# Kernel optimization log

Measured on AMD Instinct MI355X. Metric: run time of the kernel, lower is better.

## Reference

```python
import jax, jax.numpy as jnp
import numpy as np

B, S, D, H = 4, 2048, 1024, 16
HD = D // H

def setup_inputs() -> dict:
    key = jax.random.key(0)
    ks = jax.random.split(key, 11)
    s = 1.0 / np.sqrt(D)
    return {
        "query": jax.random.normal(ks[0], (B, S, D), jnp.float32),
        "key_": jax.random.normal(ks[1], (B, S, D), jnp.float32),
        "value": jax.random.normal(ks[2], (B, S, D), jnp.float32),
        "Wq": jax.random.normal(ks[3], (D, D), jnp.float32) * s,
        "bq": jax.random.normal(ks[4], (D,), jnp.float32) * s,
        "Wk": jax.random.normal(ks[5], (D, D), jnp.float32) * s,
        "bk": jax.random.normal(ks[6], (D,), jnp.float32) * s,
        "Wv": jax.random.normal(ks[7], (D, D), jnp.float32) * s,
        "bv": jax.random.normal(ks[8], (D,), jnp.float32) * s,
        "Wo": jax.random.normal(ks[9], (D, D), jnp.float32) * s,
        "bo": jax.random.normal(ks[10], (D,), jnp.float32) * s,
    }

def reference(query, key_, value, Wq, bq, Wk, bk, Wv, bv, Wo, bo):
    # projections (torch Linear: x @ W.T + b)
    q = query @ Wq.T + bq
    k = key_ @ Wk.T + bk
    v = value @ Wv.T + bv
    # [B,S,D] -> [B,H,S,hd]
    q = q.reshape(B, S, H, HD).transpose(0, 2, 1, 3)
    k = k.reshape(B, S, H, HD).transpose(0, 2, 1, 3)
    v = v.reshape(B, S, H, HD).transpose(0, 2, 1, 3)
    scale = HD ** 0.5
    scores = jnp.einsum('bhqd,bhkd->bhqk', q, k) / scale
    attn = jax.nn.softmax(scores, axis=-1)
    out = jnp.einsum('bhqk,bhkd->bhqd', attn, v)
    out = out.transpose(0, 2, 1, 3).reshape(B, S, D)
    return out @ Wo.T + bo
```

## Files before the change

kernel.cpp:

```cpp
#include <hip/hip_runtime.h>
#include <math.h>

#define B_ 4
#define S_ 2048
#define D_ 1024
#define H_ 16
#define HD_ 64
#define M_ (B_*S_)
#define BH_ (B_*H_)

typedef __attribute__((ext_vector_type(4))) float f32x4;
typedef _Float16 f16;
typedef __attribute__((ext_vector_type(8))) _Float16 f16x8;
typedef __attribute__((ext_vector_type(2))) __fp16 fp16x2_raw;
typedef unsigned short u16;

#define QSCALE 0.18033688011112042f

__device__ __forceinline__ unsigned pkh(float a, float b) {
    fp16x2_raw h = __builtin_amdgcn_cvt_pkrtz(a, b);
    unsigned r; __builtin_memcpy(&r, &h, 4);
    return r;
}
__device__ __forceinline__ uint2 f4_to_h4(float4 v) {
    uint2 r;
    r.x = pkh(v.x, v.y);
    r.y = pkh(v.z, v.w);
    return r;
}
__device__ __forceinline__ void gload_lds16(const void* g, void* l) {
    __builtin_amdgcn_global_load_lds(
        (const __attribute__((address_space(1))) void*)g,
        (__attribute__((address_space(3))) void*)l, 16, 0, 0);
}
#define MFMA16(a,b,c) __builtin_amdgcn_mfma_f32_16x16x32_f16((a),(b),(c),0,0,0)

__global__ __launch_bounds__(256) void conv_w_kernel(
    const float* __restrict__ w0, const float* __restrict__ w1,
    const float* __restrict__ w2, const float* __restrict__ w3,
    f16* __restrict__ out)
{
    const float* src = (blockIdx.y==0)?w0:(blockIdx.y==1)?w1:(blockIdx.y==2)?w2:w3;
    size_t off = (size_t)blockIdx.y << 20;
    size_t i = ((size_t)blockIdx.x*256 + threadIdx.x)*4;
    float4 v = *(const float4*)&src[i];
    *(uint2*)&out[off + i] = f4_to_h4(v);
}

__global__ __launch_bounds__(256) void conv_in_kernel(
    const float* __restrict__ src, f16* __restrict__ out)
{
    size_t i = ((size_t)blockIdx.x*256 + threadIdx.x)*4;
    float4 v = *(const float4*)&src[i];
    *(uint2*)&out[i] = f4_to_h4(v);
}

template<int MODE>
__global__ __launch_bounds__(256, 2) void gemm_mfma(
    const f16* __restrict__ Af16,
    const f16* __restrict__ Wh16,
    const float* __restrict__ bias,
    void* out0)
{
    __shared__ u16 Ah[128][32];
    __shared__ u16 Bh[128][32];

    const int t = threadIdx.x;
    const int lane = t & 63;
    const int w = t >> 6;
    const int wm = w >> 1, wn = w & 1;
    const int m0 = (int)(blockIdx.x >> 3) * 128;
    const int n0 = (int)(blockIdx.x & 7) * 128;

    const int srow_base = w*32;
    const int lrow_off  = lane >> 2;
    const int k8        = (lane & 3) * 8;

    f32x4 acc[4][4];
    #pragma unroll
    for (int i = 0; i < 4; ++i)
        #pragma unroll
        for (int j = 0; j < 4; ++j) { f32x4 z = {0.f,0.f,0.f,0.f}; acc[i][j] = z; }

    for (int k0 = 0; k0 < D_; k0 += 32) {
        __syncthreads();
        #pragma unroll
        for (int c = 0; c < 2; ++c) {
            int lrow = srow_base + c*16;
            int row = lrow + lrow_off;
            int kw = k8 ^ ((row & 3) << 3);
            size_t asrc;
            if constexpr (MODE == 3) {
                int m = m0 + row;
                int b = m >> 11, s = m & 2047;
                int kk = k0 + kw;
                asrc = (((size_t)b*H_ + (kk >> 6))*S_ + s)*HD_ + (kk & 63);
            } else {
                asrc = (size_t)(m0 + row)*D_ + k0 + kw;
            }
            gload_lds16(&Af16[asrc], &Ah[lrow][0]);
            gload_lds16(&Wh16[(size_t)(n0 + row)*D_ + k0 + kw], &Bh[lrow][0]);
        }
        __syncthreads();

        f16x8 ah[4], bh4[4];
        #pragma unroll
        for (int i = 0; i < 4; ++i) {
            int ml = wm*64 + i*16 + (lane & 15);
            int kwa = ((lane >> 4) * 8) ^ ((ml & 3) << 3);
            ah[i] = *(const f16x8*)&Ah[ml][kwa];
            int nl = wn*64 + i*16 + (lane & 15);
            int kwb = ((lane >> 4) * 8) ^ ((nl & 3) << 3);
            bh4[i] = *(const f16x8*)&Bh[nl][kwb];
        }
        __builtin_amdgcn_s_setprio(1);
        #pragma unroll
        for (int i = 0; i < 4; ++i)
            #pragma unroll
            for (int j = 0; j < 4; ++j)
                acc[i][j] = MFMA16(ah[i], bh4[j], acc[i][j]);
        __builtin_amdgcn_s_setprio(0);
    }

    #pragma unroll
    for (int i = 0; i < 4; ++i) {
        #pragma unroll
        for (int j = 0; j < 4; ++j) {
            int n = n0 + wn*64 + j*16 + (lane & 15);
            float bb = bias[n];
            int mbase = m0 + wm*64 + i*16 + (lane >> 4)*4;
            if constexpr (MODE == 3) {
                float* o = (float*)out0;
                #pragma unroll
                for (int r = 0; r < 4; ++r)
                    o[(size_t)(mbase + r)*D_ + n] = acc[i][j][r] + bb;
            } else if constexpr (MODE == 0) {
                f16* q = (f16*)out0;
                int b = mbase >> 11, h = n >> 6, hd = n & 63;
                size_t bh = (size_t)b*H_ + h;
                #pragma unroll
                for (int r = 0; r < 4; ++r) {
                    int s = (mbase + r) & 2047;
                    q[(bh*S_ + s)*64 + hd] = (f16)((acc[i][j][r] + bb) * QSCALE);
                }
            } else if constexpr (MODE == 1) {
                f16* oh = (f16*)out0;
                int b = mbase >> 11, h = n >> 6, hd = n & 63;
                size_t bh = (size_t)b*H_ + h;
                #pragma unroll
                for (int r = 0; r < 4; ++r) {
                    int s = (mbase + r) & 2047;
                    oh[(bh*S_ + s)*64 + hd] = (f16)(acc[i][j][r] + bb);
                }
            } else {
                int b = mbase >> 11, h = n >> 6, hd = n & 63;
                int s0 = mbase & 2047;
                uint2 ph;
                ph.x = pkh(acc[i][j][0] + bb, acc[i][j][1] + bb);
                ph.y = pkh(acc[i][j][2] + bb, acc[i][j][3] + bb);
                size_t idx = (((size_t)b*H_ + h)*HD_ + hd)*S_ + s0;
                *(uint2*)&((f16*)out0)[idx] = ph;
            }
        }
    }
}

__global__ __launch_bounds__(256, 2) void attn_mfma(
    const f16* __restrict__ kf,
    const f16* __restrict__ vtf,
    f16* qf)
{
    __shared__ u16 Kh[64][64];
    __shared__ u16 Vth[64][64];
    __shared__ u16 Ps[256][64];

    const int t = threadIdx.x;
    const int lane = t & 63;
    const int w = t >> 6;
    const int g = lane >> 4;
    const int l15 = lane & 15;

    const int lb = (int)blockIdx.x;
    const int logical = (lb & 7) * 64 + (lb >> 3);
    const int qtile = logical & 7;
    const int bh = logical >> 3;
    const size_t rowb = (size_t)bh * S_;
    const int q0 = qtile * 256;

    f16x8 qh[4][2];
    {
        int qr = q0 + w*64 + l15;
        #pragma unroll
        for (int mi = 0; mi < 4; ++mi)
            #pragma unroll
            for (int kk = 0; kk < 2; ++kk) {
                int d0 = kk*32 + g*8;
                qh[mi][kk] = *(const f16x8*)&qf[(rowb + qr + mi*16)*64 + d0];
            }
    }

    f32x4 O[4][4];
    float lsum[4] = {0.f, 0.f, 0.f, 0.f};
    #pragma unroll
    for (int mi = 0; mi < 4; ++mi)
        #pragma unroll
        for (int oj = 0; oj < 4; ++oj) { f32x4 z = {0.f,0.f,0.f,0.f}; O[mi][oj] = z; }

    for (int kt = 0; kt < S_/64; ++kt) {
        __syncthreads();
        #pragma unroll
        for (int c = 0; c < 2; ++c) {
            int lrow = w*16 + c*8;
            int row = lrow + (lane >> 3);
            int d8 = (lane & 7) * 8;
            int dsw = d8 ^ ((row & 7) << 3);
            size_t kg = (rowb + kt*64 + row)*64 + dsw;
            size_t vg = ((size_t)bh*HD_ + row)*S_ + kt*64 + dsw;
            gload_lds16(&kf[kg],  &Kh[lrow][0]);
            gload_lds16(&vtf[vg], &Vth[lrow][0]);
        }
        __syncthreads();

        f32x4 sa[4][4];
        #pragma unroll
        for (int k4 = 0; k4 < 4; ++k4)
            #pragma unroll
            for (int qt = 0; qt < 4; ++qt) { f32x4 z = {0.f,0.f,0.f,0.f}; sa[k4][qt] = z; }
        #pragma unroll
        for (int kk = 0; kk < 2; ++kk) {
            f16x8 kb[4];
            #pragma unroll
            for (int k4 = 0; k4 < 4; ++k4) {
                int kv = k4*16 + l15;
                int dw = (kk*32 + g*8) ^ ((kv & 7) << 3);
                kb[k4] = *(const f16x8*)&Kh[kv][dw];
            }
            __builtin_amdgcn_s_setprio(1);
            #pragma unroll
            for (int k4 = 0; k4 < 4; ++k4)
                #pragma unroll
                for (int qt = 0; qt < 4; ++qt)
                    sa[k4][qt] = MFMA16(kb[k4], qh[qt][kk], sa[k4][qt]);
            __builtin_amdgcn_s_setprio(0);
        }

        u16* Pflat = &Ps[0][0];
        #pragma unroll
        for (int qt = 0; qt < 4; ++qt) {
            int qw = w*64 + qt*16 + l15;
            int prow = qw * 64;
            int sw = (qw & 7) << 3;
            #pragma unroll
            for (int k4 = 0; k4 < 4; ++k4) {
                float p0 = exp2f(sa[k4][qt][0]);
                float p1 = exp2f(sa[k4][qt][1]);
                float p2 = exp2f(sa[k4][qt][2]);
                float p3 = exp2f(sa[k4][qt][3]);
                lsum[qt] += (p0 + p1) + (p2 + p3);
                uint2 pk;
                pk.x = pkh(p0, p1);
                pk.y = pkh(p2, p3);
                int kvb = k4*16 + g*4;
                *(uint2*)&Pflat[prow + (kvb ^ sw)] = pk;
            }
        }

        #pragma unroll
        for (int k2 = 0; k2 < 2; ++k2) {
            f16x8 pa[4], vb[4];
            #pragma unroll
            for (int mi = 0; mi < 4; ++mi) {
                int q = w*64 + mi*16 + l15;
                int kw = (k2*32 + g*8) ^ ((q & 7) << 3);
                pa[mi] = *(const f16x8*)&Pflat[q*64 + kw];
            }
            #pragma unroll
            for (int oj = 0; oj < 4; ++oj) {
                int hd = oj*16 + l15;
                int kw = (k2*32 + g*8) ^ ((hd & 7) << 3);
                vb[oj] = *(const f16x8*)&Vth[hd][kw];
            }
            __builtin_amdgcn_s_setprio(1);
            #pragma unroll
            for (int mi = 0; mi < 4; ++mi)
                #pragma unroll
                for (int oj = 0; oj < 4; ++oj)
                    O[mi][oj] = MFMA16(pa[mi], vb[oj], O[mi][oj]);
            __builtin_amdgcn_s_setprio(0);
        }
    }

    float inv[4];
    #pragma unroll
    for (int qt = 0; qt < 4; ++qt) {
        float l = lsum[qt];
        l += __shfl_xor(l, 16, 64);
        l += __shfl_xor(l, 32, 64);
        inv[qt] = 1.f / l;
    }
    #pragma unroll
    for (int mi = 0; mi < 4; ++mi)
        #pragma unroll
        for (int r = 0; r < 4; ++r) {
            float iv = __shfl(inv[mi], g*4 + r, 64);
            int q = q0 + w*64 + mi*16 + g*4 + r;
            #pragma unroll
            for (int oj = 0; oj < 4; ++oj) {
                int hd = oj*16 + l15;
                qf[(rowb + q)*HD_ + hd] = (f16)(O[mi][oj][r] * iv);
            }
        }
}

extern "C" void kernel_launch(void* const* d_in, const int* in_sizes, int n_in,
                              void* d_out, int out_size, void* d_ws, size_t ws_size,
                              hipStream_t stream) {
    const float* query = (const float*)d_in[0];
    const float* key_  = (const float*)d_in[1];
    const float* value = (const float*)d_in[2];
    const float* Wq    = (const float*)d_in[3];
    const float* bq    = (const float*)d_in[4];
    const float* Wk    = (const float*)d_in[5];
    const float* bk    = (const float*)d_in[6];
    const float* Wv    = (const float*)d_in[7];
    const float* bv    = (const float*)d_in[8];
    const float* Wo    = (const float*)d_in[9];
    const float* bo    = (const float*)d_in[10];
    float* out = (float*)d_out;

    char* wsb = (char*)d_ws;
    const size_t SZ_H = (size_t)BH_*S_*64*2;
    f16* qf   = (f16*)wsb;
    f16* kf   = (f16*)(wsb + SZ_H);
    f16* vtf  = (f16*)(wsb + 2*SZ_H);
    f16* in16 = (f16*)(wsb + 3*SZ_H);
    f16* W16  = (f16*)(wsb + 4*SZ_H);

    dim3 gGemm(512);
    dim3 gAttn(512);
    dim3 gConv(8192);

    conv_w_kernel<<<dim3(1024,4), 256, 0, stream>>>(Wq, Wk, Wv, Wo, W16);
    conv_in_kernel<<<gConv, 256, 0, stream>>>(query, in16);
    gemm_mfma<0><<<gGemm, 256, 0, stream>>>(in16, W16 + ((size_t)0<<20), bq, qf);
    conv_in_kernel<<<gConv, 256, 0, stream>>>(key_, in16);
    gemm_mfma<1><<<gGemm, 256, 0, stream>>>(in16, W16 + ((size_t)1<<20), bk, kf);
    conv_in_kernel<<<gConv, 256, 0, stream>>>(value, in16);
    gemm_mfma<2><<<gGemm, 256, 0, stream>>>(in16, W16 + ((size_t)2<<20), bv, vtf);
    attn_mfma<<<gAttn, 256, 0, stream>>>(kf, vtf, qf);
    gemm_mfma<3><<<gGemm, 256, 0, stream>>>(qf, W16 + ((size_t)3<<20), bo, out);
}
```

Baseline: 257.6 us.

## Double-buffer K/V tiles in attention kernel to overlap loads with MFMA

Splits the K and V shared-memory tiles into two buffers and issues the async global-to-LDS loads for the next key tile before computing on the current one. A partial vmcnt wait stands in for the full sync, so load latency can hide behind the QK and PV MFMAs. It costs an extra 16KB of LDS per block, which may reduce occupancy at launch_bounds(256,2). It also relies on manual waitcnt and barrier placement being correct.

Result: no change. 258.1 us (+0.2%).

```diff
diff --git a/kernel.cpp b/kernel.cpp
--- a/kernel.cpp
+++ b/kernel.cpp
@@ -170,8 +170,8 @@
     const f16* __restrict__ vtf,
     f16* qf)
 {
-    __shared__ u16 Kh[64][64];
-    __shared__ u16 Vth[64][64];
+    __shared__ u16 Kh[2][64][64];
+    __shared__ u16 Vth[2][64][64];
     __shared__ u16 Ps[256][64];
 
     const int t = threadIdx.x;
@@ -187,6 +187,9 @@
     const size_t rowb = (size_t)bh * S_;
     const int q0 = qtile * 256;
 
+    const int srow_off = lane >> 3;
+    const int sd8      = (lane & 7) * 8;
+
     f16x8 qh[4][2];
     {
         int qr = q0 + w*64 + l15;
@@ -206,20 +209,31 @@
         #pragma unroll
         for (int oj = 0; oj < 4; ++oj) { f32x4 z = {0.f,0.f,0.f,0.f}; O[mi][oj] = z; }
 
-    for (int kt = 0; kt < S_/64; ++kt) {
-        __syncthreads();
-        #pragma unroll
-        for (int c = 0; c < 2; ++c) {
-            int lrow = w*16 + c*8;
-            int row = lrow + (lane >> 3);
-            int d8 = (lane & 7) * 8;
-            int dsw = d8 ^ ((row & 7) << 3);
-            size_t kg = (rowb + kt*64 + row)*64 + dsw;
-            size_t vg = ((size_t)bh*HD_ + row)*S_ + kt*64 + dsw;
-            gload_lds16(&kf[kg],  &Kh[lrow][0]);
-            gload_lds16(&vtf[vg], &Vth[lrow][0]);
-        }
-        __syncthreads();
+#define STAGE_KV(bsel, kt_) do { \
+        _Pragma("unroll") \
+        for (int c = 0; c < 2; ++c) { \
+            int lrow = w*16 + c*8; \
+            int row = lrow + srow_off; \
+            int dsw = sd8 ^ ((row & 7) << 3); \
+            size_t kg = (rowb + (kt_)*64 + row)*64 + dsw; \
+            size_t vg = ((size_t)bh*HD_ + row)*S_ + (kt_)*64 + dsw; \
+            gload_lds16(&kf[kg],  &Kh[bsel][lrow][0]); \
+            gload_lds16(&vtf[vg], &Vth[bsel][lrow][0]); \
+        } \
+    } while (0)
+
+    STAGE_KV(0, 0);
+
+    const int NT = S_/64;
+    for (int kt = 0; kt < NT; ++kt) {
+        const int cur = kt & 1;
+        if (kt + 1 < NT) {
+            STAGE_KV(cur ^ 1, kt + 1);
+            asm volatile("s_waitcnt vmcnt(4)" ::: "memory");
+        } else {
+            asm volatile("s_waitcnt vmcnt(0)" ::: "memory");
+        }
+        __builtin_amdgcn_s_barrier();
 
         f32x4 sa[4][4];
         #pragma unroll
@@ -233,7 +247,7 @@
             for (int k4 = 0; k4 < 4; ++k4) {
                 int kv = k4*16 + l15;
                 int dw = (kk*32 + g*8) ^ ((kv & 7) << 3);
-                kb[k4] = *(const f16x8*)&Kh[kv][dw];
+                kb[k4] = *(const f16x8*)&Kh[cur][kv][dw];
             }
             __builtin_amdgcn_s_setprio(1);
             #pragma unroll
@@ -278,7 +292,7 @@
             for (int oj = 0; oj < 4; ++oj) {
                 int hd = oj*16 + l15;
                 int kw = (k2*32 + g*8) ^ ((hd & 7) << 3);
-                vb[oj] = *(const f16x8*)&Vth[hd][kw];
+                vb[oj] = *(const f16x8*)&Vth[cur][hd][kw];
             }
             __builtin_amdgcn_s_setprio(1);
             #pragma unroll
@@ -288,7 +302,10 @@
                     O[mi][oj] = MFMA16(pa[mi], vb[oj], O[mi][oj]);
             __builtin_amdgcn_s_setprio(0);
         }
-    }
+
+        __builtin_amdgcn_s_barrier();
+    }
+#undef STAGE_KV
 
     float inv[4];
     #pragma unroll
```

## Halve attention query tile to 128 rows and compute row sums via MFMA

Applied to the files above, without the earlier changes.

The attention kernel now processes 128 query rows per block instead of 256, doubling the grid to 1024 blocks and halving per-wave accumulator state and shared P buffer. The softmax denominator is accumulated with an extra MFMA against a ones vector from the fp16 P tile instead of scalar adds plus cross-lane shuffles. The first QK MFMA uses a zero accumulator directly. This trades more K/V tile reloads per query for better occupancy and parallelism, and the row sum now uses fp16-rounded probabilities.

Measured after the change: 259.0 us. About the same (+0.5%).

```diff
diff --git a/kernel.cpp b/kernel.cpp
--- a/kernel.cpp
+++ b/kernel.cpp
@@ -172,7 +172,7 @@
 {
     __shared__ u16 Kh[64][64];
     __shared__ u16 Vth[64][64];
-    __shared__ u16 Ps[256][64];
+    __shared__ u16 Ps[128][64];
 
     const int t = threadIdx.x;
     const int lane = t & 63;
@@ -181,17 +181,20 @@
     const int l15 = lane & 15;
 
     const int lb = (int)blockIdx.x;
-    const int logical = (lb & 7) * 64 + (lb >> 3);
-    const int qtile = logical & 7;
-    const int bh = logical >> 3;
+    const int logical = (lb & 7) * 128 + (lb >> 3);
+    const int qtile = logical & 15;
+    const int bh = logical >> 4;
     const size_t rowb = (size_t)bh * S_;
-    const int q0 = qtile * 256;
-
-    f16x8 qh[4][2];
+    const int q0 = qtile * 128;
+
+    const int srow_off = lane >> 3;
+    const int sd8      = (lane & 7) * 8;
+
+    f16x8 qh[2][2];
     {
-        int qr = q0 + w*64 + l15;
-        #pragma unroll
-        for (int mi = 0; mi < 4; ++mi)
+        int qr = q0 + w*32 + l15;
+        #pragma unroll
+        for (int mi = 0; mi < 2; ++mi)
             #pragma unroll
             for (int kk = 0; kk < 2; ++kk) {
                 int d0 = kk*32 + g*8;
@@ -199,21 +202,27 @@
             }
     }
 
-    f32x4 O[4][4];
-    float lsum[4] = {0.f, 0.f, 0.f, 0.f};
-    #pragma unroll
-    for (int mi = 0; mi < 4; ++mi)
-        #pragma unroll
-        for (int oj = 0; oj < 4; ++oj) { f32x4 z = {0.f,0.f,0.f,0.f}; O[mi][oj] = z; }
+    const f32x4 zero4 = {0.f, 0.f, 0.f, 0.f};
+    f16x8 ones8;
+    #pragma unroll
+    for (int e = 0; e < 8; ++e) ones8[e] = (f16)1.0f;
+
+    f32x4 O[2][4];
+    f32x4 lacc[2];
+    #pragma unroll
+    for (int mi = 0; mi < 2; ++mi) {
+        lacc[mi] = zero4;
+        #pragma unroll
+        for (int oj = 0; oj < 4; ++oj) O[mi][oj] = zero4;
+    }
 
     for (int kt = 0; kt < S_/64; ++kt) {
         __syncthreads();
         #pragma unroll
         for (int c = 0; c < 2; ++c) {
             int lrow = w*16 + c*8;
-            int row = lrow + (lane >> 3);
-            int d8 = (lane & 7) * 8;
-            int dsw = d8 ^ ((row & 7) << 3);
+            int row = lrow + srow_off;
+            int dsw = sd8 ^ ((row & 7) << 3);
             size_t kg = (rowb + kt*64 + row)*64 + dsw;
             size_t vg = ((size_t)bh*HD_ + row)*S_ + kt*64 + dsw;
             gload_lds16(&kf[kg],  &Kh[lrow][0]);
@@ -221,33 +230,44 @@
         }
         __syncthreads();
 
-        f32x4 sa[4][4];
-        #pragma unroll
-        for (int k4 = 0; k4 < 4; ++k4)
-            #pragma unroll
-            for (int qt = 0; qt < 4; ++qt) { f32x4 z = {0.f,0.f,0.f,0.f}; sa[k4][qt] = z; }
-        #pragma unroll
-        for (int kk = 0; kk < 2; ++kk) {
+        f32x4 sa[4][2];
+        {
             f16x8 kb[4];
             #pragma unroll
             for (int k4 = 0; k4 < 4; ++k4) {
                 int kv = k4*16 + l15;
-                int dw = (kk*32 + g*8) ^ ((kv & 7) << 3);
+                int dw = (g*8) ^ ((kv & 7) << 3);
                 kb[k4] = *(const f16x8*)&Kh[kv][dw];
             }
             __builtin_amdgcn_s_setprio(1);
             #pragma unroll
             for (int k4 = 0; k4 < 4; ++k4)
                 #pragma unroll
-                for (int qt = 0; qt < 4; ++qt)
-                    sa[k4][qt] = MFMA16(kb[k4], qh[qt][kk], sa[k4][qt]);
+                for (int qt = 0; qt < 2; ++qt)
+                    sa[k4][qt] = MFMA16(kb[k4], qh[qt][0], zero4);
             __builtin_amdgcn_s_setprio(0);
         }
+        {
+            f16x8 kb[4];
+            #pragma unroll
+            for (int k4 = 0; k4 < 4; ++k4) {
+                int kv = k4*16 + l15;
+                int dw = (32 + g*8) ^ ((kv & 7) << 3);
+                kb[k4] = *(const f16x8*)&Kh[kv][dw];
+            }
+            __builtin_amdgcn_s_setprio(1);
+            #pragma unroll
+            for (int k4 = 0; k4 < 4; ++k4)
+                #pragma unroll
+                for (int qt = 0; qt < 2; ++qt)
+                    sa[k4][qt] = MFMA16(kb[k4], qh[qt][1], sa[k4][qt]);
+            __builtin_amdgcn_s_setprio(0);
+        }
 
         u16* Pflat = &Ps[0][0];
         #pragma unroll
-        for (int qt = 0; qt < 4; ++qt) {
-            int qw = w*64 + qt*16 + l15;
+        for (int qt = 0; qt < 2; ++qt) {
+            int qw = w*32 + qt*16 + l15;
             int prow = qw * 64;
             int sw = (qw & 7) << 3;
             #pragma unroll
@@ -256,7 +276,6 @@
                 float p1 = exp2f(sa[k4][qt][1]);
                 float p2 = exp2f(sa[k4][qt][2]);
                 float p3 = exp2f(sa[k4][qt][3]);
-                lsum[qt] += (p0 + p1) + (p2 + p3);
                 uint2 pk;
                 pk.x = pkh(p0, p1);
                 pk.y = pkh(p2, p3);
@@ -267,10 +286,10 @@
 
         #pragma unroll
         for (int k2 = 0; k2 < 2; ++k2) {
-            f16x8 pa[4], vb[4];
-            #pragma unroll
-            for (int mi = 0; mi < 4; ++mi) {
-                int q = w*64 + mi*16 + l15;
+            f16x8 pa[2], vb[4];
+            #pragma unroll
+            for (int mi = 0; mi < 2; ++mi) {
+                int q = w*32 + mi*16 + l15;
                 int kw = (k2*32 + g*8) ^ ((q & 7) << 3);
                 pa[mi] = *(const f16x8*)&Pflat[q*64 + kw];
             }
@@ -282,28 +301,22 @@
             }
             __builtin_amdgcn_s_setprio(1);
             #pragma unroll
-            for (int mi = 0; mi < 4; ++mi)
+            for (int mi = 0; mi < 2; ++mi) {
                 #pragma unroll
                 for (int oj = 0; oj < 4; ++oj)
                     O[mi][oj] = MFMA16(pa[mi], vb[oj], O[mi][oj]);
+                lacc[mi] = MFMA16(pa[mi], ones8, lacc[mi]);
+            }
             __builtin_amdgcn_s_setprio(0);
         }
     }
 
-    float inv[4];
-    #pragma unroll
-    for (int qt = 0; qt < 4; ++qt) {
-        float l = lsum[qt];
-        l += __shfl_xor(l, 16, 64);
-        l += __shfl_xor(l, 32, 64);
-        inv[qt] = 1.f / l;
-    }
-    #pragma unroll
-    for (int mi = 0; mi < 4; ++mi)
+    #pragma unroll
+    for (int mi = 0; mi < 2; ++mi)
         #pragma unroll
         for (int r = 0; r < 4; ++r) {
-            float iv = __shfl(inv[mi], g*4 + r, 64);
-            int q = q0 + w*64 + mi*16 + g*4 + r;
+            float iv = 1.f / lacc[mi][r];
+            int q = q0 + w*32 + mi*16 + g*4 + r;
             #pragma unroll
             for (int oj = 0; oj < 4; ++oj) {
                 int hd = oj*16 + l15;
@@ -337,7 +350,7 @@
     f16* W16  = (f16*)(wsb + 4*SZ_H);
 
     dim3 gGemm(512);
-    dim3 gAttn(512);
+    dim3 gAttn(1024);
     dim3 gConv(8192);
 
     conv_w_kernel<<<dim3(1024,4), 256, 0, stream>>>(Wq, Wk, Wv, Wo, W16);
```

## Switch attention kernel from 16x16x32 to 32x32x16 MFMA tiles

Applied to the files above, without the earlier changes.

Rewrites the attention inner loops (QK^T and PV) to use 32x32x16 f16 MFMA instructions instead of 16x16x32, reshaping Q/K/V/P fragment loads and accumulator layouts. Fewer, larger MFMAs per tile are meant to raise matrix-core throughput and cut the number of LDS fragment reads. The row-sum normalization now goes through shared memory with extra barriers, and the output write pattern changes.

New measurement: 251.8 us. 1.02x faster.

```diff
diff --git a/kernel.cpp b/kernel.cpp
--- a/kernel.cpp
+++ b/kernel.cpp
@@ -10,6 +10,7 @@
 #define BH_ (B_*H_)
 
 typedef __attribute__((ext_vector_type(4))) float f32x4;
+typedef __attribute__((ext_vector_type(16))) float f32x16;
 typedef _Float16 f16;
 typedef __attribute__((ext_vector_type(8))) _Float16 f16x8;
 typedef __attribute__((ext_vector_type(2))) __fp16 fp16x2_raw;
@@ -34,6 +35,7 @@
         (__attribute__((address_space(3))) void*)l, 16, 0, 0);
 }
 #define MFMA16(a,b,c) __builtin_amdgcn_mfma_f32_16x16x32_f16((a),(b),(c),0,0,0)
+#define MFMA32(a,b,c) __builtin_amdgcn_mfma_f32_32x32x16_f16((a),(b),(c),0,0,0)
 
 __global__ __launch_bounds__(256) void conv_w_kernel(
     const float* __restrict__ w0, const float* __restrict__ w1,
@@ -173,12 +175,13 @@
     __shared__ u16 Kh[64][64];
     __shared__ u16 Vth[64][64];
     __shared__ u16 Ps[256][64];
+    __shared__ float Linv[256];
 
     const int t = threadIdx.x;
     const int lane = t & 63;
     const int w = t >> 6;
-    const int g = lane >> 4;
-    const int l15 = lane & 15;
+    const int l31 = lane & 31;
+    const int h5 = lane >> 5;
 
     const int lb = (int)blockIdx.x;
     const int logical = (lb & 7) * 64 + (lb >> 3);
@@ -187,33 +190,36 @@
     const size_t rowb = (size_t)bh * S_;
     const int q0 = qtile * 256;
 
-    f16x8 qh[4][2];
+    const int srow_off = lane >> 3;
+    const int sd8      = (lane & 7) * 8;
+
+    f16x8 qh[2][4];
     {
-        int qr = q0 + w*64 + l15;
-        #pragma unroll
-        for (int mi = 0; mi < 4; ++mi)
-            #pragma unroll
-            for (int kk = 0; kk < 2; ++kk) {
-                int d0 = kk*32 + g*8;
-                qh[mi][kk] = *(const f16x8*)&qf[(rowb + qr + mi*16)*64 + d0];
-            }
+        int qr = q0 + w*64 + l31;
+        #pragma unroll
+        for (int qt = 0; qt < 2; ++qt)
+            #pragma unroll
+            for (int dsl = 0; dsl < 4; ++dsl)
+                qh[qt][dsl] = *(const f16x8*)&qf[(rowb + qr + qt*32)*64 + dsl*16 + h5*8];
     }
 
-    f32x4 O[4][4];
-    float lsum[4] = {0.f, 0.f, 0.f, 0.f};
-    #pragma unroll
-    for (int mi = 0; mi < 4; ++mi)
-        #pragma unroll
-        for (int oj = 0; oj < 4; ++oj) { f32x4 z = {0.f,0.f,0.f,0.f}; O[mi][oj] = z; }
+    f32x16 O[2][2];
+    float lsum[2] = {0.f, 0.f};
+    f32x16 zero16;
+    #pragma unroll
+    for (int e = 0; e < 16; ++e) zero16[e] = 0.f;
+    #pragma unroll
+    for (int qt = 0; qt < 2; ++qt)
+        #pragma unroll
+        for (int ht = 0; ht < 2; ++ht) O[qt][ht] = zero16;
 
     for (int kt = 0; kt < S_/64; ++kt) {
         __syncthreads();
         #pragma unroll
         for (int c = 0; c < 2; ++c) {
             int lrow = w*16 + c*8;
-            int row = lrow + (lane >> 3);
-            int d8 = (lane & 7) * 8;
-            int dsw = d8 ^ ((row & 7) << 3);
+            int row = lrow + srow_off;
+            int dsw = sd8 ^ ((row & 7) << 3);
             size_t kg = (rowb + kt*64 + row)*64 + dsw;
             size_t vg = ((size_t)bh*HD_ + row)*S_ + kt*64 + dsw;
             gload_lds16(&kf[kg],  &Kh[lrow][0]);
@@ -221,93 +227,91 @@
         }
         __syncthreads();
 
-        f32x4 sa[4][4];
-        #pragma unroll
-        for (int k4 = 0; k4 < 4; ++k4)
-            #pragma unroll
-            for (int qt = 0; qt < 4; ++qt) { f32x4 z = {0.f,0.f,0.f,0.f}; sa[k4][qt] = z; }
-        #pragma unroll
-        for (int kk = 0; kk < 2; ++kk) {
-            f16x8 kb[4];
-            #pragma unroll
-            for (int k4 = 0; k4 < 4; ++k4) {
-                int kv = k4*16 + l15;
-                int dw = (kk*32 + g*8) ^ ((kv & 7) << 3);
-                kb[k4] = *(const f16x8*)&Kh[kv][dw];
+        f32x16 sa[2][2];
+        #pragma unroll
+        for (int dsl = 0; dsl < 4; ++dsl) {
+            f16x8 kb[2];
+            #pragma unroll
+            for (int kvt = 0; kvt < 2; ++kvt) {
+                int kv = kvt*32 + l31;
+                kb[kvt] = *(const f16x8*)&Kh[kv][(dsl*16 + h5*8) ^ ((kv & 7) << 3)];
             }
             __builtin_amdgcn_s_setprio(1);
             #pragma unroll
-            for (int k4 = 0; k4 < 4; ++k4)
-                #pragma unroll
-                for (int qt = 0; qt < 4; ++qt)
-                    sa[k4][qt] = MFMA16(kb[k4], qh[qt][kk], sa[k4][qt]);
+            for (int kvt = 0; kvt < 2; ++kvt)
+                #pragma unroll
+                for (int qt = 0; qt < 2; ++qt) {
+                    if (dsl == 0) sa[kvt][qt] = MFMA32(kb[kvt], qh[qt][0], zero16);
+                    else          sa[kvt][qt] = MFMA32(kb[kvt], qh[qt][dsl], sa[kvt][qt]);
+                }
             __builtin_amdgcn_s_setprio(0);
         }
 
         u16* Pflat = &Ps[0][0];
         #pragma unroll
-        for (int qt = 0; qt < 4; ++qt) {
-            int qw = w*64 + qt*16 + l15;
-            int prow = qw * 64;
-            int sw = (qw & 7) << 3;
-            #pragma unroll
-            for (int k4 = 0; k4 < 4; ++k4) {
-                float p0 = exp2f(sa[k4][qt][0]);
-                float p1 = exp2f(sa[k4][qt][1]);
-                float p2 = exp2f(sa[k4][qt][2]);
-                float p3 = exp2f(sa[k4][qt][3]);
-                lsum[qt] += (p0 + p1) + (p2 + p3);
-                uint2 pk;
-                pk.x = pkh(p0, p1);
-                pk.y = pkh(p2, p3);
-                int kvb = k4*16 + g*4;
-                *(uint2*)&Pflat[prow + (kvb ^ sw)] = pk;
-            }
-        }
-
-        #pragma unroll
-        for (int k2 = 0; k2 < 2; ++k2) {
-            f16x8 pa[4], vb[4];
-            #pragma unroll
-            for (int mi = 0; mi < 4; ++mi) {
-                int q = w*64 + mi*16 + l15;
-                int kw = (k2*32 + g*8) ^ ((q & 7) << 3);
-                pa[mi] = *(const f16x8*)&Pflat[q*64 + kw];
-            }
-            #pragma unroll
-            for (int oj = 0; oj < 4; ++oj) {
-                int hd = oj*16 + l15;
-                int kw = (k2*32 + g*8) ^ ((hd & 7) << 3);
-                vb[oj] = *(const f16x8*)&Vth[hd][kw];
+        for (int qt = 0; qt < 2; ++qt) {
+            int qrow = w*64 + qt*32 + l31;
+            int prow = qrow * 64;
+            int sw = (qrow & 7) << 3;
+            #pragma unroll
+            for (int kvt = 0; kvt < 2; ++kvt)
+                #pragma unroll
+                for (int quad = 0; quad < 4; ++quad) {
+                    float p0 = exp2f(sa[kvt][qt][quad*4+0]);
+                    float p1 = exp2f(sa[kvt][qt][quad*4+1]);
+                    float p2 = exp2f(sa[kvt][qt][quad*4+2]);
+                    float p3 = exp2f(sa[kvt][qt][quad*4+3]);
+                    lsum[qt] += (p0 + p1) + (p2 + p3);
+                    uint2 pk;
+                    pk.x = pkh(p0, p1);
+                    pk.y = pkh(p2, p3);
+                    int kvb = kvt*32 + quad*8 + h5*4;
+                    *(uint2*)&Pflat[prow + (kvb ^ sw)] = pk;
+                }
+        }
+
+        #pragma unroll
+        for (int ksl = 0; ksl < 4; ++ksl) {
+            f16x8 pa[2], vb[2];
+            #pragma unroll
+            for (int qt = 0; qt < 2; ++qt) {
+                int q = w*64 + qt*32 + l31;
+                pa[qt] = *(const f16x8*)&Pflat[q*64 + ((ksl*16 + h5*8) ^ ((q & 7) << 3))];
+            }
+            #pragma unroll
+            for (int ht = 0; ht < 2; ++ht) {
+                int hd = ht*32 + l31;
+                vb[ht] = *(const f16x8*)&Vth[hd][(ksl*16 + h5*8) ^ ((hd & 7) << 3)];
             }
             __builtin_amdgcn_s_setprio(1);
             #pragma unroll
-            for (int mi = 0; mi < 4; ++mi)
-                #pragma unroll
-                for (int oj = 0; oj < 4; ++oj)
-                    O[mi][oj] = MFMA16(pa[mi], vb[oj], O[mi][oj]);
+            for (int qt = 0; qt < 2; ++qt)
+                #pragma unroll
+                for (int ht = 0; ht < 2; ++ht)
+                    O[qt][ht] = MFMA32(pa[qt], vb[ht], O[qt][ht]);
             __builtin_amdgcn_s_setprio(0);
         }
     }
 
-    float inv[4];
-    #pragma unroll
-    for (int qt = 0; qt < 4; ++qt) {
-        float l = lsum[qt];
-        l += __shfl_xor(l, 16, 64);
-        l += __shfl_xor(l, 32, 64);
-        inv[qt] = 1.f / l;
-    }
-    #pragma unroll
-    for (int mi = 0; mi < 4; ++mi)
-        #pragma unroll
-        for (int r = 0; r < 4; ++r) {
-            float iv = __shfl(inv[mi], g*4 + r, 64);
-            int q = q0 + w*64 + mi*16 + g*4 + r;
-            #pragma unroll
-            for (int oj = 0; oj < 4; ++oj) {
-                int hd = oj*16 + l15;
-                qf[(rowb + q)*HD_ + hd] = (f16)(O[mi][oj][r] * iv);
+    #pragma unroll
+    for (int qt = 0; qt < 2; ++qt)
+        lsum[qt] += __shfl_xor(lsum[qt], 32, 64);
+    __syncthreads();
+    #pragma unroll
+    for (int qt = 0; qt < 2; ++qt)
+        Linv[w*64 + qt*32 + l31] = 1.f / lsum[qt];
+    __syncthreads();
+
+    #pragma unroll
+    for (int qt = 0; qt < 2; ++qt)
+        #pragma unroll
+        for (int ht = 0; ht < 2; ++ht) {
+            int hd = ht*32 + l31;
+            #pragma unroll
+            for (int reg = 0; reg < 16; ++reg) {
+                int qloc = w*64 + qt*32 + (reg & 3) + 8*(reg >> 2) + 4*h5;
+                float iv = Linv[qloc];
+                qf[(rowb + q0 + qloc)*64 + hd] = (f16)(O[qt][ht][reg] * iv);
             }
         }
 }
```
